# Kernel tuning notes

Hardware: AMD Instinct MI355X
Metric: run time of the kernel (lower is better)

The kernel has to match this reference:

```python
import jax, jax.numpy as jnp
import numpy as np
import math

B, S, D, H = 4, 1024, 1024, 16
DK = D // H


def setup_inputs() -> dict:
    key = jax.random.key(0)
    ks = jax.random.split(key, 13)
    s = 1.0 / math.sqrt(D)
    inp = {
        "query": jax.random.normal(ks[0], (B, S, D), jnp.float32),
        "key": jax.random.normal(ks[1], (B, S, D), jnp.float32),
        "value": jax.random.normal(ks[2], (B, S, D), jnp.float32),
        "mask": jax.random.randint(ks[3], (B, S, S), 0, 2, jnp.int32),
        "wq": jax.random.normal(ks[4], (D, D), jnp.float32) * s,
        "bq": jax.random.normal(ks[5], (D,), jnp.float32) * s,
        "wk": jax.random.normal(ks[6], (D, D), jnp.float32) * s,
        "bk": jax.random.normal(ks[7], (D,), jnp.float32) * s,
        "wv": jax.random.normal(ks[8], (D, D), jnp.float32) * s,
        "bv": jax.random.normal(ks[9], (D,), jnp.float32) * s,
        "wo": jax.random.normal(ks[10], (D, D), jnp.float32) * s,
        "bo": jax.random.normal(ks[11], (D,), jnp.float32) * s,
    }
    return inp


def reference(query, key, value, mask, wq, bq, wk, bk, wv, bv, wo, bo):
    # QKV projections, split into heads: [B,S,D] -> [B,H,S,DK]
    def proj(x, w, b):
        return (x @ w.T + b).reshape(B, S, H, DK).transpose(0, 2, 1, 3)

    q = proj(query, wq, bq)
    k = proj(key, wk, bk)
    v = proj(value, wv, bv)

    scores = jnp.einsum("bhqd,bhkd->bhqk", q, k) / math.sqrt(DK)
    scores = scores + mask[:, None, :, :].astype(scores.dtype) * (-1e9)
    p = jax.nn.softmax(scores, axis=-1)
    x = jnp.einsum("bhqk,bhkd->bhqd", p, v)
    x = x.transpose(0, 2, 1, 3).reshape(B, S, D)
    # output projection (dropout is identity in eval)
    return x @ wo.T + bo
```

## Files before the change

kernel.cpp:

```cpp
#include <hip/hip_runtime.h>
#include <hip/hip_bf16.h>


typedef __bf16 bf16x8 __attribute__((ext_vector_type(8)));
typedef float f32x4 __attribute__((ext_vector_type(4)));
typedef unsigned short us8 __attribute__((ext_vector_type(8)));
typedef unsigned short us4 __attribute__((ext_vector_type(4)));

#define MFMA(a, b, c) __builtin_amdgcn_mfma_f32_16x16x32_bf16(a, b, c, 0, 0, 0)
#define EXP2(x) __builtin_amdgcn_exp2f(x)

__device__ __forceinline__ unsigned short f2b(float f) {
  return __builtin_bit_cast(unsigned short, __float2bfloat16(f));
}
__device__ __forceinline__ float b2f(unsigned short u) {
  return __builtin_bit_cast(float, (unsigned)u << 16);
}
__device__ __forceinline__ unsigned cvtpk(float lo, float hi) {
  unsigned r;
  asm("v_cvt_pk_bf16_f32 %0, %1, %2" : "=v"(r) : "v"(lo), "v"(hi));
  return r;
}
__device__ __forceinline__ bf16x8 ldbf8(const unsigned short* p) {
  return __builtin_bit_cast(bf16x8, *reinterpret_cast<const us8*>(p));
}
__device__ __forceinline__ us8 cvt8(float4 a, float4 b) {
  us8 o;
  o[0] = f2b(a.x); o[1] = f2b(a.y); o[2] = f2b(a.z); o[3] = f2b(a.w);
  o[4] = f2b(b.x); o[5] = f2b(b.y); o[6] = f2b(b.z); o[7] = f2b(b.w);
  return o;
}
__device__ __forceinline__ void glds16(const void* g, void* l) {
  __builtin_amdgcn_global_load_lds(
      (const __attribute__((address_space(1))) unsigned int*)g,
      (__attribute__((address_space(3))) unsigned int*)l, 16, 0, 0);
}

__global__ __launch_bounds__(256)
void prep(const float* __restrict__ query, const float* __restrict__ key,
          const float* __restrict__ value, const float* __restrict__ wq,
          const float* __restrict__ wk, const float* __restrict__ wv,
          unsigned short* __restrict__ Abfq, unsigned short* __restrict__ Abfk,
          unsigned short* __restrict__ Abfv, unsigned short* __restrict__ Wb) {
  const int bid = blockIdx.x, tid = threadIdx.x;
  const float* src;
  unsigned short* dst;
  size_t off;
  if (bid < 1536) {
    const int widx = bid >> 9;
    src = (widx == 0) ? wq : (widx == 1) ? wk : wv;
    dst = Wb + (size_t)widx * 1048576;
    off = (size_t)(bid & 511) * 2048 + tid * 8;
  } else if (bid < 3584) {
    src = query; dst = Abfq; off = (size_t)(bid - 1536) * 2048 + tid * 8;
  } else if (bid < 5632) {
    src = key; dst = Abfk; off = (size_t)(bid - 3584) * 2048 + tid * 8;
  } else {
    src = value; dst = Abfv; off = (size_t)(bid - 5632) * 2048 + tid * 8;
  }
  const float4* p = reinterpret_cast<const float4*>(src + off);
  *reinterpret_cast<us8*>(dst + off) = cvt8(p[0], p[1]);
}

__global__ __launch_bounds__(256)
void maskcvt(const int* __restrict__ mask, unsigned short* __restrict__ Mf) {
  const int idx = blockIdx.x * 256 + threadIdx.x;
  const int wl = idx & 63, tile = idx >> 6;
  const int kt = tile & 63, qt = (tile >> 6) & 63, b = tile >> 12;
  const int lr = wl & 15, lg = wl >> 4;
  const int4 mv = *reinterpret_cast<const int4*>(
      mask + (size_t)(b * 1024 + qt * 16 + lr) * 1024 + kt * 16 + lg * 4);
  us4 o;
  o[0] = mv.x ? 0xCEACu : 0xC1C0u;
  o[1] = mv.y ? 0xCEACu : 0xC1C0u;
  o[2] = mv.z ? 0xCEACu : 0xC1C0u;
  o[3] = mv.w ? 0xCEACu : 0xC1C0u;
  *reinterpret_cast<us4*>(Mf + (size_t)idx * 4) = o;
}

__global__ __launch_bounds__(256)
void cvt_w(const float* __restrict__ src, unsigned short* __restrict__ dst) {
  const size_t off = (size_t)blockIdx.x * 2048 + threadIdx.x * 8;
  const float4* p = reinterpret_cast<const float4*>(src + off);
  *reinterpret_cast<us8*>(dst + off) = cvt8(p[0], p[1]);
}

__global__ __launch_bounds__(512, 6)
void gemm_proj(const unsigned short* __restrict__ Aq,
               const unsigned short* __restrict__ Ak,
               const unsigned short* __restrict__ Av_bf,
               const float* __restrict__ Av_f32,
               const unsigned short* __restrict__ Wb,
               const float* __restrict__ bq, const float* __restrict__ bk,
               const float* __restrict__ bv, unsigned short* __restrict__ Qb,
               unsigned short* __restrict__ Kf, unsigned short* __restrict__ Vf,
               float qscale) {
  constexpr int K = 1024, N = 1024;
  __shared__ __align__(16) unsigned short As[2][128 * 32];
  __shared__ __align__(16) unsigned short Bs[2][128 * 32];
  const int lid = blockIdx.x + (blockIdx.y << 5) + (blockIdx.z << 8);
  const int xcd = lid & 7, slot = lid >> 3;
  const int chunk = ((slot >> 3) << 3) + xcd;
  const int z = chunk >> 5;
  const int bm = (chunk & 31) * 128;
  const int bn = (slot & 7) * 128;

  const unsigned short* Abf = (z == 0) ? Aq : (z == 1) ? Ak : Av_bf;
  const bool f32path = (z == 2) && (Av_bf == nullptr);
  const unsigned short* Bw = Wb + (size_t)z * 1048576;
  const float* bias = (z == 0) ? bq : (z == 1) ? bk : bv;
  const int t = threadIdx.x;
  const int w = t >> 6, lane = t & 63, lr = lane & 15, lg = lane >> 4;
  const int wr = w >> 2, wc = w & 3;

  const int sline = t >> 3;
  const int su = (t & 7) ^ (sline & 7);
  const int srow = sline * 2 + (su >> 2);
  const int scol = (su & 3) * 8;

  f32x4 acc[4][2];
#pragma unroll
  for (int m = 0; m < 4; ++m)
#pragma unroll
    for (int n = 0; n < 2; ++n) acc[m][n] = f32x4{0.f, 0.f, 0.f, 0.f};

  auto stageA = [&](int k0, int buf) {
    const char* g = (const char*)(Abf + (size_t)(bm + srow) * 1024 + k0 + scol);
    char* l = (char*)&As[buf][0] + (w * 64) * 16;
    glds16(g, l);
  };
  auto stageB = [&](int k0, int buf) {
    const char* g = (const char*)(Bw + (size_t)(bn + srow) * 1024 + k0 + scol);
    char* l = (char*)&Bs[buf][0] + (w * 64) * 16;
    glds16(g, l);
  };
#define STA8(buf, v)                                                           \
  { *reinterpret_cast<us8*>((char*)&As[buf][0] + t * 16) = (v); }

#define RDOFF(row) (((row) >> 1) * 128 +                                       \
                    (((lg | (((row) & 1) << 2)) ^ (((row) >> 1) & 7)) * 16))

  if (f32path) {
    const float4* p =
        reinterpret_cast<const float4*>(Av_f32 + (size_t)(bm + srow) * K + scol);
    STA8(0, cvt8(p[0], p[1]));
  } else {
    stageA(0, 0);
  }
  stageB(0, 0);
  __syncthreads();

  for (int c = 0; c < 32; ++c) {
    const int buf = c & 1;
    float4 fa[2];
    if (c < 31) {
      const int k1 = (c + 1) * 32;
      if (f32path) {
        const float4* p = reinterpret_cast<const float4*>(
            Av_f32 + (size_t)(bm + srow) * K + k1 + scol);
        fa[0] = p[0];
        fa[1] = p[1];
      } else {
        stageA(k1, buf ^ 1);
      }
      stageB(k1, buf ^ 1);
    }
    {
      bf16x8 af[4], bfr[2];
#pragma unroll
      for (int m = 0; m < 4; ++m) {
        const int row = wr * 64 + m * 16 + lr;
        af[m] = ldbf8((const unsigned short*)((char*)&As[buf][0] + RDOFF(row)));
      }
#pragma unroll
      for (int n = 0; n < 2; ++n) {
        const int row = wc * 32 + n * 16 + lr;
        bfr[n] = ldbf8((const unsigned short*)((char*)&Bs[buf][0] + RDOFF(row)));
      }
#pragma unroll
      for (int m = 0; m < 4; ++m)
#pragma unroll
        for (int n = 0; n < 2; ++n) acc[m][n] = MFMA(af[m], bfr[n], acc[m][n]);
    }
    if (c < 31 && f32path) {
      STA8(buf ^ 1, cvt8(fa[0], fa[1]));
    }
    __syncthreads();
  }
#undef STA8
#undef RDOFF

#pragma unroll
  for (int m = 0; m < 4; ++m) {
    const int mr = bm + wr * 64 + m * 16 + lg * 4;
#pragma unroll
    for (int nt = 0; nt < 2; ++nt) {
      const int n = bn + wc * 32 + nt * 16 + lr;
      const float bb = bias[n];
      if (z == 0) {
#pragma unroll
        for (int r = 0; r < 4; ++r)
          Qb[(size_t)(mr + r) * N + n] = f2b((acc[m][nt][r] + bb) * qscale);
      } else if (z == 1) {
        const int b2 = mr >> 10, s0 = mr & 1023, hh = n >> 6, dd = n & 63;
        const size_t base = (size_t)(b2 * 16 + hh) * 65536 + (size_t)(dd >> 5) * 32768 +
                            (size_t)(s0 >> 4) * 512 +
                            (size_t)((s0 & 15) | (((dd >> 3) & 3) << 4)) * 8 + (dd & 7);
#pragma unroll
        for (int r = 0; r < 4; ++r) Kf[base + r * 8] = f2b(acc[m][nt][r] + bb);
      } else {
        const int b2 = mr >> 10, s0 = mr & 1023, hh = n >> 6, dd = n & 63;
        const size_t base = (size_t)(b2 * 16 + hh) * 65536 + (size_t)(s0 >> 5) * 2048 +
                            (size_t)(dd >> 4) * 512 +
                            (size_t)((dd & 15) | (((s0 >> 3) & 3) << 4)) * 8 + (s0 & 7);
        us4 pk;
#pragma unroll
        for (int r = 0; r < 4; ++r) pk[r] = f2b(acc[m][nt][r] + bb);
        *reinterpret_cast<us4*>(&Vf[base]) = pk;
      }
    }
  }
}

__global__ __launch_bounds__(256)
void gemm_out(const unsigned short* __restrict__ A, const unsigned short* __restrict__ Bw,
              const float* __restrict__ bias, float* __restrict__ Out) {
  constexpr int K = 1024, N = 1024;
  __shared__ __align__(16) unsigned short As[2][128 * 64];
  __shared__ __align__(16) unsigned short Bs[2][64 * 64];
  const int lid = blockIdx.x + (blockIdx.y << 5);
  const int xcd = lid & 7, slot = lid >> 3;
  const int chunk = ((slot >> 5) << 3) + xcd;
  const int pos = slot & 31;
  const int bm = ((chunk << 1) + (pos >> 4)) * 128;
  const int bn = (pos & 15) * 64;
  const int t = threadIdx.x;
  const int w = t >> 6, lane = t & 63, lr = lane & 15, lg = lane >> 4;
  const int wr = w >> 1, wc = w & 1;
  const int swzc = (lr & 7) << 4;

  f32x4 acc[4][2];
#pragma unroll
  for (int m = 0; m < 4; ++m)
#pragma unroll
    for (int n = 0; n < 2; ++n) acc[m][n] = f32x4{0.f, 0.f, 0.f, 0.f};

  auto stageA = [&](int k0, int buf) {
#pragma unroll
    for (int it = 0; it < 4; ++it) {
      const int s = it * 256 + t, row = s >> 3, cb = (s & 7) * 16;
      const char* g = (const char*)A + ((size_t)(bm + row) * 1024 + k0) * 2 +
                      (cb ^ ((row & 7) << 4));
      char* l = (char*)&As[buf][0] + (it * 256 + w * 64) * 16;
      glds16(g, l);
    }
  };
  auto stageB = [&](int k0, int buf) {
#pragma unroll
    for (int it = 0; it < 2; ++it) {
      const int s = it * 256 + t, row = s >> 3, cb = (s & 7) * 16;
      const char* g = (const char*)Bw + ((size_t)(bn + row) * 1024 + k0) * 2 +
                      (cb ^ ((row & 7) << 4));
      char* l = (char*)&Bs[buf][0] + (it * 256 + w * 64) * 16;
      glds16(g, l);
    }
  };

  stageA(0, 0);
  stageB(0, 0);
  __syncthreads();

  for (int c = 0; c < 16; ++c) {
    const int buf = c & 1;
    if (c < 15) {
      const int k1 = (c + 1) * 64;
      stageA(k1, buf ^ 1);
      stageB(k1, buf ^ 1);
    }
#pragma unroll
    for (int h2 = 0; h2 < 2; ++h2) {
      bf16x8 af[4], bfr[2];
#pragma unroll
      for (int m = 0; m < 4; ++m) {
        const int row = wr * 64 + m * 16 + lr;
        af[m] = ldbf8((const unsigned short*)((char*)&As[buf][0] + row * 128 +
                                              ((h2 * 64 + lg * 16) ^ swzc)));
      }
#pragma unroll
      for (int n = 0; n < 2; ++n) {
        const int row = wc * 32 + n * 16 + lr;
        bfr[n] = ldbf8((const unsigned short*)((char*)&Bs[buf][0] + row * 128 +
                                               ((h2 * 64 + lg * 16) ^ swzc)));
      }
#pragma unroll
      for (int m = 0; m < 4; ++m)
#pragma unroll
        for (int n = 0; n < 2; ++n) acc[m][n] = MFMA(af[m], bfr[n], acc[m][n]);
    }
    __syncthreads();
  }

#pragma unroll
  for (int m = 0; m < 4; ++m) {
    const int mr = bm + wr * 64 + m * 16 + lg * 4;
#pragma unroll
    for (int nt = 0; nt < 2; ++nt) {
      const int n = bn + wc * 32 + nt * 16 + lr;
      const float bb = bias[n];
#pragma unroll
      for (int r = 0; r < 4; ++r) Out[(size_t)(mr + r) * N + n] = acc[m][nt][r] + bb;
    }
  }
}

__global__ __launch_bounds__(256)
void attn_v7(const unsigned short* __restrict__ Qb,
             const unsigned short* __restrict__ Kf,
             const unsigned short* __restrict__ Vf,
             const unsigned short* __restrict__ Mf,
             unsigned short* __restrict__ ctx) {
  __shared__ __align__(16) unsigned short S[2][8192];
  __shared__ __align__(16) unsigned short sP[4][16 * 64];
  const int lid = blockIdx.x + (blockIdx.y << 6);
  const int xcd = lid & 7, slot = lid >> 3;
  const int bh = ((slot >> 4) << 3) + xcd;
  const int qb = slot & 15;
  const int b = bh >> 4, h = bh & 15;
  const int t = threadIdx.x, w = t >> 6, wl = t & 63, lr = wl & 15, lg = wl >> 4;
  const int q0 = qb * 64 + w * 16;
  const int swz = (lr & 7) << 4;

  const unsigned short* qp = Qb + (size_t)(b * 1024 + q0 + lr) * 1024 + h * 64 + lg * 8;
  const bf16x8 bq0 = ldbf8(qp);
  const bf16x8 bq1 = ldbf8(qp + 32);

  const unsigned short* KfB = Kf + (size_t)bh * 65536;
  const unsigned short* VfB = Vf + (size_t)bh * 65536;
  const unsigned short* mfp = Mf + (size_t)((b * 64 + qb * 4 + w) * 64) * 256 + wl * 4;

  f32x4 O[4];
  float l_ = 0.f;
#pragma unroll
  for (int dt = 0; dt < 4; ++dt) O[dt] = f32x4{0.f, 0.f, 0.f, 0.f};
  unsigned short* sp = &sP[w][0];

  auto stage = [&](int kc, int buf) {
    const unsigned short* srcs[4] = {KfB + kc * 2048, KfB + 32768 + kc * 2048,
                                     VfB + kc * 4096, VfB + kc * 4096 + 2048};
#pragma unroll
    for (int r = 0; r < 4; ++r) {
      const char* g = (const char*)(srcs[r] + (size_t)t * 8);
      char* l = (char*)&S[buf][r * 2048 + w * 512];
      glds16(g, l);
    }
  };

  stage(0, 0);
  __syncthreads();

  for (int kc = 0; kc < 16; ++kc) {
    const int buf = kc & 1;
    if (kc < 15) stage(kc + 1, buf ^ 1);

    us4 mk[4];
#pragma unroll
    for (int t4 = 0; t4 < 4; ++t4)
      mk[t4] = *reinterpret_cast<const us4*>(mfp + (size_t)(kc * 4 + t4) * 256);

    bf16x8 ak[4][2];
#pragma unroll
    for (int t4 = 0; t4 < 4; ++t4) {
      ak[t4][0] = ldbf8(&S[buf][t4 * 512 + wl * 8]);
      ak[t4][1] = ldbf8(&S[buf][2048 + t4 * 512 + wl * 8]);
    }

    f32x4 sc[4];
    __builtin_amdgcn_s_setprio(1);
#pragma unroll
    for (int t4 = 0; t4 < 4; ++t4) {
      f32x4 a;
#pragma unroll
      for (int r = 0; r < 4; ++r) a[r] = b2f(mk[t4][r]);
      a = MFMA(ak[t4][0], bq0, a);
      a = MFMA(ak[t4][1], bq1, a);
      sc[t4] = a;
    }
    __builtin_amdgcn_s_setprio(0);

    float ps = 0.f;
#pragma unroll
    for (int t4 = 0; t4 < 4; ++t4) {
      const float e0 = EXP2(sc[t4][0]), e1 = EXP2(sc[t4][1]);
      const float e2 = EXP2(sc[t4][2]), e3 = EXP2(sc[t4][3]);
      ps += (e0 + e1) + (e2 + e3);
      uint2 pw;
      pw.x = cvtpk(e0, e1);
      pw.y = cvtpk(e2, e3);
      *reinterpret_cast<uint2*>((char*)sp + lr * 128 + ((t4 * 32 + lg * 8) ^ swz)) = pw;
    }
    ps += __shfl_xor(ps, 16);
    ps += __shfl_xor(ps, 32);
    l_ += ps;

    __builtin_amdgcn_s_setprio(1);
#pragma unroll
    for (int ks = 0; ks < 2; ++ks) {
      bf16x8 ap =
          ldbf8((const unsigned short*)((char*)sp + lr * 128 + ((ks * 64 + lg * 16) ^ swz)));
#pragma unroll
      for (int dt = 0; dt < 4; ++dt) {
        bf16x8 bv = ldbf8(&S[buf][4096 + ks * 2048 + dt * 512 + wl * 8]);
        O[dt] = MFMA(ap, bv, O[dt]);
      }
    }
    __builtin_amdgcn_s_setprio(0);

    __syncthreads();
  }

  float linv[4];
#pragma unroll
  for (int r = 0; r < 4; ++r) linv[r] = 1.0f / __shfl(l_, lg * 4 + r);
#pragma unroll
  for (int dt = 0; dt < 4; ++dt)
#pragma unroll
    for (int r = 0; r < 4; ++r)
      ctx[(size_t)(b * 1024 + q0 + lg * 4 + r) * 1024 + h * 64 + dt * 16 + lr] =
          f2b(O[dt][r] * linv[r]);
}

extern "C" void kernel_launch(void* const* d_in, const int* in_sizes, int n_in,
                              void* d_out, int out_size, void* d_ws, size_t ws_size,
                              hipStream_t stream) {
  const float* query = (const float*)d_in[0];
  const float* key   = (const float*)d_in[1];
  const float* value = (const float*)d_in[2];
  const int*   mask  = (const int*)d_in[3];
  const float* wq = (const float*)d_in[4];
  const float* bq = (const float*)d_in[5];
  const float* wk = (const float*)d_in[6];
  const float* bk = (const float*)d_in[7];
  const float* wv = (const float*)d_in[8];
  const float* bv = (const float*)d_in[9];
  const float* wo = (const float*)d_in[10];
  const float* bo = (const float*)d_in[11];
  float* out = (float*)d_out;

  const size_t SZ = (size_t)4096 * 1024;
  unsigned short* Qb   = (unsigned short*)d_ws;
  unsigned short* Kf   = Qb + SZ;
  unsigned short* Vf   = Kf + SZ;
  unsigned short* ctx  = Vf + SZ;
  unsigned short* Abfq = (unsigned short*)d_out;
  unsigned short* Wb   = Abfq + SZ;
  unsigned short* Mf   = (unsigned short*)d_out;
  unsigned short* Abfk = ctx;
  const bool big = ws_size >= (size_t)40 * 1024 * 1024;
  unsigned short* Abfv = big ? (ctx + SZ) : nullptr;
  unsigned short* Wob  = Vf;

  const float qscale = 0.125f * 1.4426950408889634f;
  dim3 blk(256);
  prep<<<big ? 7680 : 5632, blk, 0, stream>>>(query, key, value, wq, wk, wv,
                                              Abfq, Abfk, Abfv, Wb);
  gemm_proj<<<dim3(32, 8, 3), dim3(512), 0, stream>>>(Abfq, Abfk, Abfv, value, Wb,
                                                      bq, bk, bv, Qb, Kf, Vf, qscale);
  maskcvt<<<4096, blk, 0, stream>>>(mask, Mf);
  attn_v7<<<dim3(64, 16), blk, 0, stream>>>(Qb, Kf, Vf, Mf, ctx);
  cvt_w<<<512, blk, 0, stream>>>(wo, Wob);
  gemm_out<<<dim3(32, 16), blk, 0, stream>>>(ctx, Wob, bo, out);
}
```

Baseline: 116.5 us.

## Process two query sub-tiles per wave in attention and widen output GEMM blocks

Each attention wave now handles 32 query rows as two 16-row sub-tiles. The K and V fragments staged in shared memory are reused for both, which halves K/V staging and LDS traffic per query, and the attention grid is halved. The output GEMM moves to 512-thread blocks with the same 128x64 tile, so each wave owns a smaller 32x32 sub-tile and more waves are available to hide latency. The cost is higher register pressure in attention (twice the accumulators and scores) and fewer attention blocks to fill the CUs.

```diff
diff --git a/kernel.cpp b/kernel.cpp
--- a/kernel.cpp
+++ b/kernel.cpp
@@ -136,7 +136,6 @@
   };
 #define STA8(buf, v)                                                           \
   { *reinterpret_cast<us8*>((char*)&As[buf][0] + t * 16) = (v); }
-
 #define RDOFF(row) (((row) >> 1) * 128 +                                       \
                     (((lg | (((row) & 1) << 2)) ^ (((row) >> 1) & 7)) * 16))
 
@@ -222,7 +221,7 @@
   }
 }
 
-__global__ __launch_bounds__(256)
+__global__ __launch_bounds__(512, 4)
 void gemm_out(const unsigned short* __restrict__ A, const unsigned short* __restrict__ Bw,
               const float* __restrict__ bias, float* __restrict__ Out) {
   constexpr int K = 1024, N = 1024;
@@ -239,31 +238,28 @@
   const int wr = w >> 1, wc = w & 1;
   const int swzc = (lr & 7) << 4;
 
-  f32x4 acc[4][2];
-#pragma unroll
-  for (int m = 0; m < 4; ++m)
+  f32x4 acc[2][2];
+#pragma unroll
+  for (int m = 0; m < 2; ++m)
 #pragma unroll
     for (int n = 0; n < 2; ++n) acc[m][n] = f32x4{0.f, 0.f, 0.f, 0.f};
 
   auto stageA = [&](int k0, int buf) {
 #pragma unroll
-    for (int it = 0; it < 4; ++it) {
-      const int s = it * 256 + t, row = s >> 3, cb = (s & 7) * 16;
+    for (int it = 0; it < 2; ++it) {
+      const int s = it * 512 + t, row = s >> 3, cb = (s & 7) * 16;
       const char* g = (const char*)A + ((size_t)(bm + row) * 1024 + k0) * 2 +
                       (cb ^ ((row & 7) << 4));
-      char* l = (char*)&As[buf][0] + (it * 256 + w * 64) * 16;
+      char* l = (char*)&As[buf][0] + (it * 512 + w * 64) * 16;
       glds16(g, l);
     }
   };
   auto stageB = [&](int k0, int buf) {
-#pragma unroll
-    for (int it = 0; it < 2; ++it) {
-      const int s = it * 256 + t, row = s >> 3, cb = (s & 7) * 16;
-      const char* g = (const char*)Bw + ((size_t)(bn + row) * 1024 + k0) * 2 +
-                      (cb ^ ((row & 7) << 4));
-      char* l = (char*)&Bs[buf][0] + (it * 256 + w * 64) * 16;
-      glds16(g, l);
-    }
+    const int s = t, row = s >> 3, cb = (s & 7) * 16;
+    const char* g = (const char*)Bw + ((size_t)(bn + row) * 1024 + k0) * 2 +
+                    (cb ^ ((row & 7) << 4));
+    char* l = (char*)&Bs[buf][0] + (w * 64) * 16;
+    glds16(g, l);
   };
 
   stageA(0, 0);
@@ -279,10 +275,10 @@
     }
 #pragma unroll
     for (int h2 = 0; h2 < 2; ++h2) {
-      bf16x8 af[4], bfr[2];
-#pragma unroll
-      for (int m = 0; m < 4; ++m) {
-        const int row = wr * 64 + m * 16 + lr;
+      bf16x8 af[2], bfr[2];
+#pragma unroll
+      for (int m = 0; m < 2; ++m) {
+        const int row = wr * 32 + m * 16 + lr;
         af[m] = ldbf8((const unsigned short*)((char*)&As[buf][0] + row * 128 +
                                               ((h2 * 64 + lg * 16) ^ swzc)));
       }
@@ -293,7 +289,7 @@
                                                ((h2 * 64 + lg * 16) ^ swzc)));
       }
 #pragma unroll
-      for (int m = 0; m < 4; ++m)
+      for (int m = 0; m < 2; ++m)
 #pragma unroll
         for (int n = 0; n < 2; ++n) acc[m][n] = MFMA(af[m], bfr[n], acc[m][n]);
     }
@@ -301,8 +297,8 @@
   }
 
 #pragma unroll
-  for (int m = 0; m < 4; ++m) {
-    const int mr = bm + wr * 64 + m * 16 + lg * 4;
+  for (int m = 0; m < 2; ++m) {
+    const int mr = bm + wr * 32 + m * 16 + lg * 4;
 #pragma unroll
     for (int nt = 0; nt < 2; ++nt) {
       const int n = bn + wc * 32 + nt * 16 + lr;
@@ -314,35 +310,46 @@
 }
 
 __global__ __launch_bounds__(256)
-void attn_v7(const unsigned short* __restrict__ Qb,
-             const unsigned short* __restrict__ Kf,
-             const unsigned short* __restrict__ Vf,
-             const unsigned short* __restrict__ Mf,
-             unsigned short* __restrict__ ctx) {
+void attn_v10(const unsigned short* __restrict__ Qb,
+              const unsigned short* __restrict__ Kf,
+              const unsigned short* __restrict__ Vf,
+              const unsigned short* __restrict__ Mf,
+              unsigned short* __restrict__ ctx) {
   __shared__ __align__(16) unsigned short S[2][8192];
-  __shared__ __align__(16) unsigned short sP[4][16 * 64];
+  __shared__ __align__(16) unsigned short sP[4][2][1024];
   const int lid = blockIdx.x + (blockIdx.y << 6);
   const int xcd = lid & 7, slot = lid >> 3;
-  const int bh = ((slot >> 4) << 3) + xcd;
-  const int qb = slot & 15;
+  const int bh = ((slot >> 3) << 3) + xcd;
+  const int qb = slot & 7;
   const int b = bh >> 4, h = bh & 15;
   const int t = threadIdx.x, w = t >> 6, wl = t & 63, lr = wl & 15, lg = wl >> 4;
-  const int q0 = qb * 64 + w * 16;
+  const int q0 = qb * 128 + w * 32;
   const int swz = (lr & 7) << 4;
 
-  const unsigned short* qp = Qb + (size_t)(b * 1024 + q0 + lr) * 1024 + h * 64 + lg * 8;
-  const bf16x8 bq0 = ldbf8(qp);
-  const bf16x8 bq1 = ldbf8(qp + 32);
+  bf16x8 bq[2][2];
+#pragma unroll
+  for (int qs = 0; qs < 2; ++qs) {
+    const unsigned short* qp =
+        Qb + (size_t)(b * 1024 + q0 + qs * 16 + lr) * 1024 + h * 64 + lg * 8;
+    bq[qs][0] = ldbf8(qp);
+    bq[qs][1] = ldbf8(qp + 32);
+  }
 
   const unsigned short* KfB = Kf + (size_t)bh * 65536;
   const unsigned short* VfB = Vf + (size_t)bh * 65536;
-  const unsigned short* mfp = Mf + (size_t)((b * 64 + qb * 4 + w) * 64) * 256 + wl * 4;
-
-  f32x4 O[4];
-  float l_ = 0.f;
-#pragma unroll
-  for (int dt = 0; dt < 4; ++dt) O[dt] = f32x4{0.f, 0.f, 0.f, 0.f};
-  unsigned short* sp = &sP[w][0];
+  const unsigned short* mfp[2];
+#pragma unroll
+  for (int qs = 0; qs < 2; ++qs)
+    mfp[qs] = Mf + (size_t)((b * 64 + qb * 8 + w * 2 + qs) * 64) * 256 + wl * 4;
+
+  f32x4 O[2][4];
+  float l_[2] = {0.f, 0.f};
+#pragma unroll
+  for (int qs = 0; qs < 2; ++qs)
+#pragma unroll
+    for (int dt = 0; dt < 4; ++dt) O[qs][dt] = f32x4{0.f, 0.f, 0.f, 0.f};
+  unsigned short* sp0 = &sP[w][0][0];
+  unsigned short* sp1 = &sP[w][1][0];
 
   auto stage = [&](int kc, int buf) {
     const unsigned short* srcs[4] = {KfB + kc * 2048, KfB + 32768 + kc * 2048,
@@ -362,10 +369,12 @@
     const int buf = kc & 1;
     if (kc < 15) stage(kc + 1, buf ^ 1);
 
-    us4 mk[4];
-#pragma unroll
-    for (int t4 = 0; t4 < 4; ++t4)
-      mk[t4] = *reinterpret_cast<const us4*>(mfp + (size_t)(kc * 4 + t4) * 256);
+    us4 mk[2][4];
+#pragma unroll
+    for (int qs = 0; qs < 2; ++qs)
+#pragma unroll
+      for (int t4 = 0; t4 < 4; ++t4)
+        mk[qs][t4] = *reinterpret_cast<const us4*>(mfp[qs] + (size_t)(kc * 4 + t4) * 256);
 
     bf16x8 ak[4][2];
 #pragma unroll
@@ -374,43 +383,51 @@
       ak[t4][1] = ldbf8(&S[buf][2048 + t4 * 512 + wl * 8]);
     }
 
-    f32x4 sc[4];
+    f32x4 sc[2][4];
     __builtin_amdgcn_s_setprio(1);
 #pragma unroll
-    for (int t4 = 0; t4 < 4; ++t4) {
-      f32x4 a;
-#pragma unroll
-      for (int r = 0; r < 4; ++r) a[r] = b2f(mk[t4][r]);
-      a = MFMA(ak[t4][0], bq0, a);
-      a = MFMA(ak[t4][1], bq1, a);
-      sc[t4] = a;
-    }
+    for (int qs = 0; qs < 2; ++qs)
+#pragma unroll
+      for (int t4 = 0; t4 < 4; ++t4) {
+        f32x4 a;
+#pragma unroll
+        for (int r = 0; r < 4; ++r) a[r] = b2f(mk[qs][t4][r]);
+        a = MFMA(ak[t4][0], bq[qs][0], a);
+        a = MFMA(ak[t4][1], bq[qs][1], a);
+        sc[qs][t4] = a;
+      }
     __builtin_amdgcn_s_setprio(0);
 
-    float ps = 0.f;
-#pragma unroll
-    for (int t4 = 0; t4 < 4; ++t4) {
-      const float e0 = EXP2(sc[t4][0]), e1 = EXP2(sc[t4][1]);
-      const float e2 = EXP2(sc[t4][2]), e3 = EXP2(sc[t4][3]);
-      ps += (e0 + e1) + (e2 + e3);
-      uint2 pw;
-      pw.x = cvtpk(e0, e1);
-      pw.y = cvtpk(e2, e3);
-      *reinterpret_cast<uint2*>((char*)sp + lr * 128 + ((t4 * 32 + lg * 8) ^ swz)) = pw;
-    }
-    ps += __shfl_xor(ps, 16);
-    ps += __shfl_xor(ps, 32);
-    l_ += ps;
+#pragma unroll
+    for (int qs = 0; qs < 2; ++qs) {
+      unsigned short* sp = qs ? sp1 : sp0;
+      float ps = 0.f;
+#pragma unroll
+      for (int t4 = 0; t4 < 4; ++t4) {
+        const float e0 = EXP2(sc[qs][t4][0]), e1 = EXP2(sc[qs][t4][1]);
+        const float e2 = EXP2(sc[qs][t4][2]), e3 = EXP2(sc[qs][t4][3]);
+        ps += (e0 + e1) + (e2 + e3);
+        uint2 pw;
+        pw.x = cvtpk(e0, e1);
+        pw.y = cvtpk(e2, e3);
+        *reinterpret_cast<uint2*>((char*)sp + lr * 128 + ((t4 * 32 + lg * 8) ^ swz)) = pw;
+      }
+      ps += __shfl_xor(ps, 16);
+      ps += __shfl_xor(ps, 32);
+      l_[qs] += ps;
+    }
 
     __builtin_amdgcn_s_setprio(1);
 #pragma unroll
     for (int ks = 0; ks < 2; ++ks) {
-      bf16x8 ap =
-          ldbf8((const unsigned short*)((char*)sp + lr * 128 + ((ks * 64 + lg * 16) ^ swz)));
+      const int off = lr * 128 + ((ks * 64 + lg * 16) ^ swz);
+      bf16x8 apA = ldbf8((const unsigned short*)((char*)sp0 + off));
+      bf16x8 apB = ldbf8((const unsigned short*)((char*)sp1 + off));
 #pragma unroll
       for (int dt = 0; dt < 4; ++dt) {
         bf16x8 bv = ldbf8(&S[buf][4096 + ks * 2048 + dt * 512 + wl * 8]);
-        O[dt] = MFMA(ap, bv, O[dt]);
+        O[0][dt] = MFMA(apA, bv, O[0][dt]);
+        O[1][dt] = MFMA(apB, bv, O[1][dt]);
       }
     }
     __builtin_amdgcn_s_setprio(0);
@@ -418,15 +435,18 @@
     __syncthreads();
   }
 
-  float linv[4];
-#pragma unroll
-  for (int r = 0; r < 4; ++r) linv[r] = 1.0f / __shfl(l_, lg * 4 + r);
-#pragma unroll
-  for (int dt = 0; dt < 4; ++dt)
-#pragma unroll
-    for (int r = 0; r < 4; ++r)
-      ctx[(size_t)(b * 1024 + q0 + lg * 4 + r) * 1024 + h * 64 + dt * 16 + lr] =
-          f2b(O[dt][r] * linv[r]);
+#pragma unroll
+  for (int qs = 0; qs < 2; ++qs) {
+    float linv[4];
+#pragma unroll
+    for (int r = 0; r < 4; ++r) linv[r] = 1.0f / __shfl(l_[qs], lg * 4 + r);
+#pragma unroll
+    for (int dt = 0; dt < 4; ++dt)
+#pragma unroll
+      for (int r = 0; r < 4; ++r)
+        ctx[(size_t)(b * 1024 + q0 + qs * 16 + lg * 4 + r) * 1024 + h * 64 + dt * 16 + lr] =
+            f2b(O[qs][dt][r] * linv[r]);
+  }
 }
 
 extern "C" void kernel_launch(void* const* d_in, const int* in_sizes, int n_in,
@@ -466,7 +486,7 @@
   gemm_proj<<<dim3(32, 8, 3), dim3(512), 0, stream>>>(Abfq, Abfk, Abfv, value, Wb,
                                                       bq, bk, bv, Qb, Kf, Vf, qscale);
   maskcvt<<<4096, blk, 0, stream>>>(mask, Mf);
-  attn_v7<<<dim3(64, 16), blk, 0, stream>>>(Qb, Kf, Vf, Mf, ctx);
+  attn_v10<<<dim3(64, 8), blk, 0, stream>>>(Qb, Kf, Vf, Mf, ctx);
   cvt_w<<<512, blk, 0, stream>>>(wo, Wob);
-  gemm_out<<<dim3(32, 16), blk, 0, stream>>>(ctx, Wob, bo, out);
-}
+  gemm_out<<<dim3(32, 16), dim3(512), 0, stream>>>(ctx, Wob, bo, out);
+}
```

New measurement: 114.9 us. Within noise of the previous version (-1.4%).
